# Performance work log

Measured on AMD Instinct MI355X. Metric: run time of the kernel, lower is better.

Reference implementation:

```python
import jax, jax.numpy as jnp
from jax import lax
import numpy as np

B, T, IN, H, OUT = 1024, 512, 64, 128, 2
BN_EPS = 1e-5


def _gru_layer(x, w_ih, w_hh, b_ih, b_hh):
    # x: [B, T, F]; w_ih: [3H, F]; w_hh: [3H, H]; gate order = (r, z, n) as in PyTorch
    Bb = x.shape[0]
    Hh = w_hh.shape[1]
    xg = jnp.einsum('btf,gf->btg', x, w_ih) + b_ih  # precompute input gates [B, T, 3H]

    def step(h, xg_t):
        hg = h @ w_hh.T + b_hh                       # [B, 3H]
        xr, xz, xn = jnp.split(xg_t, 3, axis=-1)
        hr, hz, hn = jnp.split(hg, 3, axis=-1)
        r = jax.nn.sigmoid(xr + hr)
        z = jax.nn.sigmoid(xz + hz)
        n = jnp.tanh(xn + r * hn)
        h_new = (1.0 - z) * n + z * h
        return h_new, h_new

    h0 = jnp.zeros((Bb, Hh), dtype=x.dtype)
    _, ys = lax.scan(step, h0, jnp.swapaxes(xg, 0, 1))  # scan over time
    return jnp.swapaxes(ys, 0, 1)                        # [B, T, H]


def setup_inputs() -> dict:
    key = jax.random.key(0)
    ks = jax.random.split(key, 16)
    s_in = 1.0 / np.sqrt(H)  # PyTorch GRU init scale
    d = {
        'x': jax.random.normal(ks[0], (B, T, IN), dtype=jnp.float32),
        'w_ih0': jax.random.uniform(ks[1], (3 * H, IN), minval=-s_in, maxval=s_in),
        'w_hh0': jax.random.uniform(ks[2], (3 * H, H), minval=-s_in, maxval=s_in),
        'b_ih0': jax.random.uniform(ks[3], (3 * H,), minval=-s_in, maxval=s_in),
        'b_hh0': jax.random.uniform(ks[4], (3 * H,), minval=-s_in, maxval=s_in),
        'w_ih1': jax.random.uniform(ks[5], (3 * H, H), minval=-s_in, maxval=s_in),
        'w_hh1': jax.random.uniform(ks[6], (3 * H, H), minval=-s_in, maxval=s_in),
        'b_ih1': jax.random.uniform(ks[7], (3 * H,), minval=-s_in, maxval=s_in),
        'b_hh1': jax.random.uniform(ks[8], (3 * H,), minval=-s_in, maxval=s_in),
        'fc1_w': jax.random.normal(ks[9], (H // 2, H)) * 0.05,
        'fc1_b': jnp.zeros((H // 2,)),
        'fc2_w': jax.random.normal(ks[10], (OUT, H // 2)) * 0.05,
        'fc2_b': jnp.zeros((OUT,)),
        'bn_gamma': jnp.ones((H // 2,)),
        'bn_beta': jnp.zeros((H // 2,)),
        'bn_mean': jnp.zeros((H // 2,)),
        'bn_var': jnp.ones((H // 2,)),
    }
    return d


def reference(x, w_ih0, w_hh0, b_ih0, b_hh0, w_ih1, w_hh1, b_ih1, b_hh1,
              fc1_w, fc1_b, fc2_w, fc2_b, bn_gamma, bn_beta, bn_mean, bn_var):
    h1 = _gru_layer(x, w_ih0, w_hh0, b_ih0, b_hh0)   # [B, T, H]
    h2 = _gru_layer(h1, w_ih1, w_hh1, b_ih1, b_hh1)  # [B, T, H]
    out = h2[:, -1, :]                                # last timestep [B, H]
    # dropout = identity (eval mode)
    out = jax.nn.relu(out @ fc1_w.T + fc1_b)          # [B, H/2]
    out = (out - bn_mean) * jax.lax.rsqrt(bn_var + BN_EPS) * bn_gamma + bn_beta
    out = out @ fc2_w.T + fc2_b                       # [B, 2]
    return out
```

## Files before the change

### kernel.cpp

```cpp
#include <hip/hip_runtime.h>
#include <hip/hip_bf16.h>

namespace {

typedef _Float16 h16;
typedef _Float16 f16x8 __attribute__((ext_vector_type(8)));
typedef _Float16 f16x4 __attribute__((ext_vector_type(4)));
typedef _Float16 f16x2 __attribute__((ext_vector_type(2)));
typedef float    f32x4 __attribute__((ext_vector_type(4)));
typedef unsigned long long u64;

constexpr int T_SEQ = 512;
constexpr int B_SZ  = 1024;
constexpr int H_DIM = 128;
constexpr int ROWS  = 16;
constexpr int NT    = 512;
constexpr int NGRP  = B_SZ / ROWS;
constexpr int CHUNK = 32;

template <int INDIM, bool PROD>
__device__ void gru_body(char* smem_raw, float* headbuf,
                         const float* __restrict__ xin,
                         const float* __restrict__ w_ih,
                         const float* __restrict__ w_hh,
                         const float* __restrict__ b_ih,
                         const float* __restrict__ b_hh,
                         u64* __restrict__ h1q,
                         int* __restrict__ flag,
                         const float* __restrict__ fc1_w,
                         const float* __restrict__ fc1_b,
                         const float* __restrict__ fc2_w,
                         const float* __restrict__ fc2_b,
                         const float* __restrict__ gamma,
                         const float* __restrict__ beta,
                         const float* __restrict__ mean,
                         const float* __restrict__ var,
                         float* __restrict__ out,
                         const int g)
{
  constexpr int KSH  = H_DIM / 32;
  constexpr int KSX  = INDIM / 32;
  constexpr int ROWP = H_DIM + INDIM + 8;

  auto hx = reinterpret_cast<h16 (*)[ROWS][ROWP]>(smem_raw);

  const int tid = threadIdx.x;
  const int wv  = tid >> 6;
  const int ln  = tid & 63;
  const int q   = ln >> 4;
  const int lr  = ln & 15;
  const int r0  = g * ROWS;
  const int j0  = wv * 16 + q * 4;

  f16x8 wA[3][KSH], wB[3][KSX];
  #pragma unroll
  for (int p = 0; p < 3; ++p) {
    const int gr = p * H_DIM + wv * 16 + lr;
    #pragma unroll
    for (int ks = 0; ks < KSH; ++ks) {
      const float* pw = w_hh + (size_t)gr * H_DIM + ks * 32 + q * 8;
      const float4 v0 = *(const float4*)(pw);
      const float4 v1 = *(const float4*)(pw + 4);
      f16x8 f;
      f[0]=(h16)v0.x; f[1]=(h16)v0.y; f[2]=(h16)v0.z; f[3]=(h16)v0.w;
      f[4]=(h16)v1.x; f[5]=(h16)v1.y; f[6]=(h16)v1.z; f[7]=(h16)v1.w;
      wA[p][ks] = f;
    }
    #pragma unroll
    for (int ks = 0; ks < KSX; ++ks) {
      const float* pw = w_ih + (size_t)gr * INDIM + ks * 32 + q * 8;
      const float4 v0 = *(const float4*)(pw);
      const float4 v1 = *(const float4*)(pw + 4);
      f16x8 f;
      f[0]=(h16)v0.x; f[1]=(h16)v0.y; f[2]=(h16)v0.z; f[3]=(h16)v0.w;
      f[4]=(h16)v1.x; f[5]=(h16)v1.y; f[6]=(h16)v1.z; f[7]=(h16)v1.w;
      wB[p][ks] = f;
    }
  }

  f32x4 bR, bZ, bNx, bNh;
  {
    const float4 ir  = *(const float4*)&b_ih[j0];
    const float4 hr  = *(const float4*)&b_hh[j0];
    const float4 iz  = *(const float4*)&b_ih[H_DIM + j0];
    const float4 hz  = *(const float4*)&b_hh[H_DIM + j0];
    const float4 in_ = *(const float4*)&b_ih[2 * H_DIM + j0];
    const float4 hn  = *(const float4*)&b_hh[2 * H_DIM + j0];
    bR[0]=ir.x+hr.x; bR[1]=ir.y+hr.y; bR[2]=ir.z+hr.z; bR[3]=ir.w+hr.w;
    bZ[0]=iz.x+hz.x; bZ[1]=iz.y+hz.y; bZ[2]=iz.z+hz.z; bZ[3]=iz.w+hz.w;
    bNx[0]=in_.x; bNx[1]=in_.y; bNx[2]=in_.z; bNx[3]=in_.w;
    bNh[0]=hn.x;  bNh[1]=hn.y;  bNh[2]=hn.z;  bNh[3]=hn.w;
  }

  const int sr = tid >> 5;
  const int si = tid & 31;

  {
    f16x4 z; z[0]=z[1]=z[2]=z[3] = (h16)0.f;
    *(f16x4*)&hx[0][sr][si * 4] = z;
  }
  f16x4 h_old; h_old[0]=h_old[1]=h_old[2]=h_old[3] = (h16)0.f;

  auto load_h1 = [&](int t, f16x4& d) {
    const u64 bits = __hip_atomic_load(&h1q[((size_t)t * NGRP + g) * 512 + tid],
                                       __ATOMIC_RELAXED, __HIP_MEMORY_SCOPE_AGENT);
    __builtin_memcpy(&d, &bits, 8);
  };

  f16x2 sA, sB;
  f16x4 cA, cB;
  if constexpr (PROD) {
    const float2 v0 = *(const float2*)(xin + ((size_t)(r0 + sr) * T_SEQ + 0) * 64 + si * 2);
    f16x2 s0; s0[0] = (h16)v0.x; s0[1] = (h16)v0.y;
    *(f16x2*)&hx[0][sr][H_DIM + si * 2] = s0;
    const float2 v1 = *(const float2*)(xin + ((size_t)(r0 + sr) * T_SEQ + 1) * 64 + si * 2);
    sA[0] = (h16)v1.x; sA[1] = (h16)v1.y;
  } else {
    while (__hip_atomic_load(flag, __ATOMIC_ACQUIRE, __HIP_MEMORY_SCOPE_AGENT) < 1)
      __builtin_amdgcn_s_sleep(2);
    f16x4 s0; load_h1(0, s0);
    *(f16x4*)&hx[0][lr][H_DIM + j0] = s0;
    load_h1(1, cA);
  }
  __syncthreads();

  auto gates = [&](const f32x4& aR, const f32x4& aZ, const f32x4& aNx2, const f32x4& aNh2,
                   f16x4& nv4, float* hnv) {
    #pragma unroll
    for (int i = 0; i < 4; ++i) {
      const float rg = __builtin_amdgcn_rcpf(1.f + __expf(-aR[i]));
      const float zg = __builtin_amdgcn_rcpf(1.f + __expf(-aZ[i]));
      const float na = aNx2[i] + rg * aNh2[i];
      const float e2 = __expf(2.f * na);
      const float ng = 1.f - 2.f * __builtin_amdgcn_rcpf(e2 + 1.f);
      const float ho = (float)h_old[i];
      const float hn = ng + zg * (ho - ng);
      hnv[i] = hn;
      nv4[i] = (h16)hn;
    }
    h_old = nv4;
  };

  auto mfma_all = [&](const f16x8* bh, const f16x8* bx,
                      f32x4& aR, f32x4& aZ, f32x4& aNh2, f32x4& aNx2) {
    aR = bR; aZ = bZ; aNh2 = bNh; aNx2 = bNx;
    #pragma unroll
    for (int ks = 0; ks < KSH; ++ks) {
      aR   = __builtin_amdgcn_mfma_f32_16x16x32_f16(wA[0][ks], bh[ks], aR, 0, 0, 0);
      aZ   = __builtin_amdgcn_mfma_f32_16x16x32_f16(wA[1][ks], bh[ks], aZ, 0, 0, 0);
      aNh2 = __builtin_amdgcn_mfma_f32_16x16x32_f16(wA[2][ks], bh[ks], aNh2, 0, 0, 0);
    }
    #pragma unroll
    for (int ks = 0; ks < KSX; ++ks) {
      aR   = __builtin_amdgcn_mfma_f32_16x16x32_f16(wB[0][ks], bx[ks], aR, 0, 0, 0);
      aZ   = __builtin_amdgcn_mfma_f32_16x16x32_f16(wB[1][ks], bx[ks], aZ, 0, 0, 0);
      aNx2 = __builtin_amdgcn_mfma_f32_16x16x32_f16(wB[2][ks], bx[ks], aNx2, 0, 0, 0);
    }
  };

  if constexpr (PROD) {
    auto pstep = [&](int t, int cur, f16x2& s_use, f16x2& s_load) {
      f16x8 bh[KSH], bx[KSX];
      #pragma unroll
      for (int ks = 0; ks < KSH; ++ks) bh[ks] = *(const f16x8*)&hx[cur][lr][ks * 32 + q * 8];
      #pragma unroll
      for (int ks = 0; ks < KSX; ++ks) bx[ks] = *(const f16x8*)&hx[cur][lr][H_DIM + ks * 32 + q * 8];

      {
        const int tt = (t + 2 < T_SEQ) ? t + 2 : T_SEQ - 1;
        const float2 v = *(const float2*)(xin + ((size_t)(r0 + sr) * T_SEQ + tt) * 64 + si * 2);
        s_load[0] = (h16)v.x; s_load[1] = (h16)v.y;
      }

      f32x4 aR, aZ, aNh2, aNx2;
      mfma_all(bh, bx, aR, aZ, aNh2, aNx2);

      f16x4 nv4; float hnv[4];
      gates(aR, aZ, aNx2, aNh2, nv4, hnv);

      u64 bits; __builtin_memcpy(&bits, &nv4, 8);
      __hip_atomic_store(&h1q[((size_t)t * NGRP + g) * 512 + tid], bits,
                         __ATOMIC_RELAXED, __HIP_MEMORY_SCOPE_AGENT);

      *(f16x4*)&hx[cur ^ 1][lr][j0] = nv4;
      *(f16x2*)&hx[cur ^ 1][sr][H_DIM + si * 2] = s_use;

      if ((t & (CHUNK - 1)) == CHUNK - 1) __threadfence();
      __syncthreads();
      if (((t & (CHUNK - 1)) == CHUNK - 1) && tid == 0)
        __hip_atomic_store(flag, (t + 1) / CHUNK, __ATOMIC_RELEASE, __HIP_MEMORY_SCOPE_AGENT);
    };

    #pragma unroll 1
    for (int t = 0; t < T_SEQ; t += 2) {
      pstep(t,     0, sA, sB);
      pstep(t + 1, 1, sB, sA);
    }
  } else {
    auto cstep = [&](int t, int cur, f16x4& s_use, f16x4& s_load) {
      f16x8 bh[KSH], bx[KSX];
      #pragma unroll
      for (int ks = 0; ks < KSH; ++ks) bh[ks] = *(const f16x8*)&hx[cur][lr][ks * 32 + q * 8];
      #pragma unroll
      for (int ks = 0; ks < KSX; ++ks) bx[ks] = *(const f16x8*)&hx[cur][lr][H_DIM + ks * 32 + q * 8];

      if (t + 2 < T_SEQ) {
        if (((t + 2) & (CHUNK - 1)) == 0) {
          const int need = (t + 2) / CHUNK + 1;
          while (__hip_atomic_load(flag, __ATOMIC_ACQUIRE, __HIP_MEMORY_SCOPE_AGENT) < need)
            __builtin_amdgcn_s_sleep(2);
        }
        load_h1(t + 2, s_load);
      }

      f32x4 aR, aZ, aNh2, aNx2;
      mfma_all(bh, bx, aR, aZ, aNh2, aNx2);

      f16x4 nv4; float hnv[4];
      gates(aR, aZ, aNx2, aNh2, nv4, hnv);

      *(f16x4*)&hx[cur ^ 1][lr][j0] = nv4;
      if (t + 1 < T_SEQ) *(f16x4*)&hx[cur ^ 1][lr][H_DIM + j0] = s_use;

      if (t == T_SEQ - 1) {
        float* h2f = headbuf;
        float* act = headbuf + 16 * 128;
        #pragma unroll
        for (int i = 0; i < 4; ++i) h2f[lr * 128 + j0 + i] = hnv[i];
        __syncthreads();
        {
          const int row = tid >> 5;
          const float* hr = &h2f[row * 128];
          #pragma unroll
          for (int half = 0; half < 2; ++half) {
            const int j = (tid & 31) + half * 32;
            float s = fc1_b[j];
            const float4* wr = (const float4*)(fc1_w + (size_t)j * H_DIM);
            #pragma unroll
            for (int k4 = 0; k4 < H_DIM / 4; ++k4) {
              const float4 w = wr[k4];
              const float4 h = ((const float4*)hr)[k4];
              s += w.x * h.x + w.y * h.y + w.z * h.z + w.w * h.w;
            }
            s = fmaxf(s, 0.f);
            s = (s - mean[j]) * rsqrtf(var[j] + 1e-5f) * gamma[j] + beta[j];
            act[row * 64 + j] = s;
          }
        }
        __syncthreads();
        if (tid < 32) {
          const int r = tid >> 1, o = tid & 1;
          float s = fc2_b[o];
          #pragma unroll
          for (int k = 0; k < 64; ++k) s += fc2_w[(size_t)o * 64 + k] * act[r * 64 + k];
          out[(size_t)(r0 + r) * 2 + o] = s;
        }
      }
      __syncthreads();
    };

    #pragma unroll 1
    for (int t = 0; t < T_SEQ; t += 2) {
      cstep(t,     0, cA, cB);
      cstep(t + 1, 1, cB, cA);
    }
  }
}

__global__ __launch_bounds__(NT, 1)
void gru_fused(const float* __restrict__ x,
               const float* __restrict__ w_ih0, const float* __restrict__ w_hh0,
               const float* __restrict__ b_ih0, const float* __restrict__ b_hh0,
               const float* __restrict__ w_ih1, const float* __restrict__ w_hh1,
               const float* __restrict__ b_ih1, const float* __restrict__ b_hh1,
               u64* __restrict__ h1q, int* __restrict__ flags,
               const float* __restrict__ fc1_w, const float* __restrict__ fc1_b,
               const float* __restrict__ fc2_w, const float* __restrict__ fc2_b,
               const float* __restrict__ gamma, const float* __restrict__ beta,
               const float* __restrict__ mean,  const float* __restrict__ var,
               float* __restrict__ out)
{
  __shared__ __align__(16) char smem[(size_t)2 * ROWS * (H_DIM + H_DIM + 8) * sizeof(h16)];
  __shared__ __align__(16) float headbuf[16 * 128 + 16 * 64];
  const int bid = blockIdx.x;
  if (bid < NGRP)
    gru_body<64, true>(smem, headbuf, x, w_ih0, w_hh0, b_ih0, b_hh0, h1q, &flags[bid],
                       nullptr, nullptr, nullptr, nullptr, nullptr, nullptr, nullptr, nullptr,
                       nullptr, bid);
  else
    gru_body<128, false>(smem, headbuf, nullptr, w_ih1, w_hh1, b_ih1, b_hh1, h1q,
                         &flags[bid - NGRP], fc1_w, fc1_b, fc2_w, fc2_b, gamma, beta,
                         mean, var, out, bid - NGRP);
}

}

extern "C" void kernel_launch(void* const* d_in, const int* in_sizes, int n_in,
                              void* d_out, int out_size, void* d_ws, size_t ws_size,
                              hipStream_t stream) {
  const float* x     = (const float*)d_in[0];
  const float* w_ih0 = (const float*)d_in[1];
  const float* w_hh0 = (const float*)d_in[2];
  const float* b_ih0 = (const float*)d_in[3];
  const float* b_hh0 = (const float*)d_in[4];
  const float* w_ih1 = (const float*)d_in[5];
  const float* w_hh1 = (const float*)d_in[6];
  const float* b_ih1 = (const float*)d_in[7];
  const float* b_hh1 = (const float*)d_in[8];
  const float* fc1_w = (const float*)d_in[9];
  const float* fc1_b = (const float*)d_in[10];
  const float* fc2_w = (const float*)d_in[11];
  const float* fc2_b = (const float*)d_in[12];
  const float* gamma = (const float*)d_in[13];
  const float* beta  = (const float*)d_in[14];
  const float* mean  = (const float*)d_in[15];
  const float* var   = (const float*)d_in[16];
  float* out = (float*)d_out;

  char* ws = (char*)d_ws;
  const size_t h1_bytes = (size_t)T_SEQ * NGRP * 512 * sizeof(u64);
  const size_t fl_bytes = (size_t)NGRP * sizeof(int);
  if (ws_size < h1_bytes + fl_bytes) return;

  u64* h1q   = (u64*)ws;
  int* flags = (int*)(ws + h1_bytes);

  hipMemsetAsync(flags, 0, fl_bytes, stream);
  gru_fused<<<dim3(2 * NGRP), dim3(NT), 0, stream>>>(
      x, w_ih0, w_hh0, b_ih0, b_hh0, w_ih1, w_hh1, b_ih1, b_hh1, h1q, flags,
      fc1_w, fc1_b, fc2_w, fc2_b, gamma, beta, mean, var, out);
}
```

Baseline: 648.2 us.

## Process two 16-row batch groups per block to interleave independent MFMA chains

```diff
diff --git a/kernel.cpp b/kernel.cpp
--- a/kernel.cpp
+++ b/kernel.cpp
@@ -16,6 +16,7 @@
 constexpr int ROWS  = 16;
 constexpr int NT    = 512;
 constexpr int NGRP  = B_SZ / ROWS;
+constexpr int NBLK  = NGRP / 2;
 constexpr int CHUNK = 32;
 
 template <int INDIM, bool PROD>
@@ -36,20 +37,22 @@
                          const float* __restrict__ mean,
                          const float* __restrict__ var,
                          float* __restrict__ out,
-                         const int g)
+                         const int gA)
 {
   constexpr int KSH  = H_DIM / 32;
   constexpr int KSX  = INDIM / 32;
   constexpr int ROWP = H_DIM + INDIM + 8;
 
-  auto hx = reinterpret_cast<h16 (*)[ROWS][ROWP]>(smem_raw);
+  auto hx = reinterpret_cast<h16 (*)[2][ROWS][ROWP]>(smem_raw);
 
   const int tid = threadIdx.x;
   const int wv  = tid >> 6;
   const int ln  = tid & 63;
   const int q   = ln >> 4;
   const int lr  = ln & 15;
-  const int r0  = g * ROWS;
+  const int gB  = gA + 1;
+  const int r0A = gA * ROWS;
+  const int r0B = gB * ROWS;
   const int j0  = wv * 16 + q * 4;
 
   f16x8 wA[3][KSH], wB[3][KSX];
@@ -97,35 +100,45 @@
 
   {
     f16x4 z; z[0]=z[1]=z[2]=z[3] = (h16)0.f;
-    *(f16x4*)&hx[0][sr][si * 4] = z;
-  }
-  f16x4 h_old; h_old[0]=h_old[1]=h_old[2]=h_old[3] = (h16)0.f;
-
-  auto load_h1 = [&](int t, f16x4& d) {
+    *(f16x4*)&hx[0][0][sr][si * 4] = z;
+    *(f16x4*)&hx[0][1][sr][si * 4] = z;
+  }
+  f16x4 h_oldA, h_oldB;
+  h_oldA[0]=h_oldA[1]=h_oldA[2]=h_oldA[3] = (h16)0.f;
+  h_oldB = h_oldA;
+
+  auto load_h1 = [&](int t, int g, f16x4& d) {
     const u64 bits = __hip_atomic_load(&h1q[((size_t)t * NGRP + g) * 512 + tid],
                                        __ATOMIC_RELAXED, __HIP_MEMORY_SCOPE_AGENT);
     __builtin_memcpy(&d, &bits, 8);
   };
-
-  f16x2 sA, sB;
-  f16x4 cA, cB;
+  auto load_x = [&](int t, int r0, f16x2& d) {
+    const int tt = (t < T_SEQ) ? t : T_SEQ - 1;
+    const float2 v = *(const float2*)(xin + ((size_t)(r0 + sr) * T_SEQ + tt) * 64 + si * 2);
+    d[0] = (h16)v.x; d[1] = (h16)v.y;
+  };
+
+  f16x2 pA_A, pA_B, pB_A, pB_B;
+  f16x4 cA_A, cA_B, cB_A, cB_B;
   if constexpr (PROD) {
-    const float2 v0 = *(const float2*)(xin + ((size_t)(r0 + sr) * T_SEQ + 0) * 64 + si * 2);
-    f16x2 s0; s0[0] = (h16)v0.x; s0[1] = (h16)v0.y;
-    *(f16x2*)&hx[0][sr][H_DIM + si * 2] = s0;
-    const float2 v1 = *(const float2*)(xin + ((size_t)(r0 + sr) * T_SEQ + 1) * 64 + si * 2);
-    sA[0] = (h16)v1.x; sA[1] = (h16)v1.y;
+    f16x2 s0;
+    load_x(0, r0A, s0); *(f16x2*)&hx[0][0][sr][H_DIM + si * 2] = s0;
+    load_x(0, r0B, s0); *(f16x2*)&hx[0][1][sr][H_DIM + si * 2] = s0;
+    load_x(1, r0A, pA_A);
+    load_x(1, r0B, pA_B);
   } else {
     while (__hip_atomic_load(flag, __ATOMIC_ACQUIRE, __HIP_MEMORY_SCOPE_AGENT) < 1)
       __builtin_amdgcn_s_sleep(2);
-    f16x4 s0; load_h1(0, s0);
-    *(f16x4*)&hx[0][lr][H_DIM + j0] = s0;
-    load_h1(1, cA);
+    f16x4 s0;
+    load_h1(0, gA, s0); *(f16x4*)&hx[0][0][lr][H_DIM + j0] = s0;
+    load_h1(0, gB, s0); *(f16x4*)&hx[0][1][lr][H_DIM + j0] = s0;
+    load_h1(1, gA, cA_A);
+    load_h1(1, gB, cA_B);
   }
   __syncthreads();
 
   auto gates = [&](const f32x4& aR, const f32x4& aZ, const f32x4& aNx2, const f32x4& aNh2,
-                   f16x4& nv4, float* hnv) {
+                   f16x4& h_old, f16x4& nv4, float* hnv) {
     #pragma unroll
     for (int i = 0; i < 4; ++i) {
       const float rg = __builtin_amdgcn_rcpf(1.f + __expf(-aR[i]));
@@ -141,49 +154,60 @@
     h_old = nv4;
   };
 
-  auto mfma_all = [&](const f16x8* bh, const f16x8* bx,
-                      f32x4& aR, f32x4& aZ, f32x4& aNh2, f32x4& aNx2) {
-    aR = bR; aZ = bZ; aNh2 = bNh; aNx2 = bNx;
-    #pragma unroll
-    for (int ks = 0; ks < KSH; ++ks) {
-      aR   = __builtin_amdgcn_mfma_f32_16x16x32_f16(wA[0][ks], bh[ks], aR, 0, 0, 0);
-      aZ   = __builtin_amdgcn_mfma_f32_16x16x32_f16(wA[1][ks], bh[ks], aZ, 0, 0, 0);
-      aNh2 = __builtin_amdgcn_mfma_f32_16x16x32_f16(wA[2][ks], bh[ks], aNh2, 0, 0, 0);
-    }
-    #pragma unroll
-    for (int ks = 0; ks < KSX; ++ks) {
-      aR   = __builtin_amdgcn_mfma_f32_16x16x32_f16(wB[0][ks], bx[ks], aR, 0, 0, 0);
-      aZ   = __builtin_amdgcn_mfma_f32_16x16x32_f16(wB[1][ks], bx[ks], aZ, 0, 0, 0);
-      aNx2 = __builtin_amdgcn_mfma_f32_16x16x32_f16(wB[2][ks], bx[ks], aNx2, 0, 0, 0);
-    }
-  };
-
   if constexpr (PROD) {
-    auto pstep = [&](int t, int cur, f16x2& s_use, f16x2& s_load) {
-      f16x8 bh[KSH], bx[KSX];
-      #pragma unroll
-      for (int ks = 0; ks < KSH; ++ks) bh[ks] = *(const f16x8*)&hx[cur][lr][ks * 32 + q * 8];
-      #pragma unroll
-      for (int ks = 0; ks < KSX; ++ks) bx[ks] = *(const f16x8*)&hx[cur][lr][H_DIM + ks * 32 + q * 8];
-
-      {
-        const int tt = (t + 2 < T_SEQ) ? t + 2 : T_SEQ - 1;
-        const float2 v = *(const float2*)(xin + ((size_t)(r0 + sr) * T_SEQ + tt) * 64 + si * 2);
-        s_load[0] = (h16)v.x; s_load[1] = (h16)v.y;
-      }
-
-      f32x4 aR, aZ, aNh2, aNx2;
-      mfma_all(bh, bx, aR, aZ, aNh2, aNx2);
-
-      f16x4 nv4; float hnv[4];
-      gates(aR, aZ, aNx2, aNh2, nv4, hnv);
-
-      u64 bits; __builtin_memcpy(&bits, &nv4, 8);
-      __hip_atomic_store(&h1q[((size_t)t * NGRP + g) * 512 + tid], bits,
+    auto pstep = [&](int t, int cur, f16x2& uA, f16x2& uB, f16x2& lA, f16x2& lB) {
+      f16x8 bhA[KSH], bxA[KSX], bhB[KSH], bxB[KSX];
+      #pragma unroll
+      for (int ks = 0; ks < KSH; ++ks) {
+        bhA[ks] = *(const f16x8*)&hx[cur][0][lr][ks * 32 + q * 8];
+        bhB[ks] = *(const f16x8*)&hx[cur][1][lr][ks * 32 + q * 8];
+      }
+      #pragma unroll
+      for (int ks = 0; ks < KSX; ++ks) {
+        bxA[ks] = *(const f16x8*)&hx[cur][0][lr][H_DIM + ks * 32 + q * 8];
+        bxB[ks] = *(const f16x8*)&hx[cur][1][lr][H_DIM + ks * 32 + q * 8];
+      }
+
+      load_x(t + 2, r0A, lA);
+      load_x(t + 2, r0B, lB);
+
+      f32x4 aRA = bR, aZA = bZ, aNhA = bNh, aNxA = bNx;
+      f32x4 aRB = bR, aZB = bZ, aNhB = bNh, aNxB = bNx;
+      #pragma unroll
+      for (int ks = 0; ks < KSH; ++ks) {
+        aRA  = __builtin_amdgcn_mfma_f32_16x16x32_f16(wA[0][ks], bhA[ks], aRA,  0, 0, 0);
+        aRB  = __builtin_amdgcn_mfma_f32_16x16x32_f16(wA[0][ks], bhB[ks], aRB,  0, 0, 0);
+        aZA  = __builtin_amdgcn_mfma_f32_16x16x32_f16(wA[1][ks], bhA[ks], aZA,  0, 0, 0);
+        aZB  = __builtin_amdgcn_mfma_f32_16x16x32_f16(wA[1][ks], bhB[ks], aZB,  0, 0, 0);
+        aNhA = __builtin_amdgcn_mfma_f32_16x16x32_f16(wA[2][ks], bhA[ks], aNhA, 0, 0, 0);
+        aNhB = __builtin_amdgcn_mfma_f32_16x16x32_f16(wA[2][ks], bhB[ks], aNhB, 0, 0, 0);
+      }
+      #pragma unroll
+      for (int ks = 0; ks < KSX; ++ks) {
+        aRA  = __builtin_amdgcn_mfma_f32_16x16x32_f16(wB[0][ks], bxA[ks], aRA,  0, 0, 0);
+        aRB  = __builtin_amdgcn_mfma_f32_16x16x32_f16(wB[0][ks], bxB[ks], aRB,  0, 0, 0);
+        aZA  = __builtin_amdgcn_mfma_f32_16x16x32_f16(wB[1][ks], bxA[ks], aZA,  0, 0, 0);
+        aZB  = __builtin_amdgcn_mfma_f32_16x16x32_f16(wB[1][ks], bxB[ks], aZB,  0, 0, 0);
+        aNxA = __builtin_amdgcn_mfma_f32_16x16x32_f16(wB[2][ks], bxA[ks], aNxA, 0, 0, 0);
+        aNxB = __builtin_amdgcn_mfma_f32_16x16x32_f16(wB[2][ks], bxB[ks], aNxB, 0, 0, 0);
+      }
+
+      f16x4 nvA, nvB; float hnA[4], hnB[4];
+      gates(aRA, aZA, aNxA, aNhA, h_oldA, nvA, hnA);
+      gates(aRB, aZB, aNxB, aNhB, h_oldB, nvB, hnB);
+
+      u64 bA, bB;
+      __builtin_memcpy(&bA, &nvA, 8);
+      __builtin_memcpy(&bB, &nvB, 8);
+      __hip_atomic_store(&h1q[((size_t)t * NGRP + gA) * 512 + tid], bA,
                          __ATOMIC_RELAXED, __HIP_MEMORY_SCOPE_AGENT);
-
-      *(f16x4*)&hx[cur ^ 1][lr][j0] = nv4;
-      *(f16x2*)&hx[cur ^ 1][sr][H_DIM + si * 2] = s_use;
+      __hip_atomic_store(&h1q[((size_t)t * NGRP + gB) * 512 + tid], bB,
+                         __ATOMIC_RELAXED, __HIP_MEMORY_SCOPE_AGENT);
+
+      *(f16x4*)&hx[cur ^ 1][0][lr][j0] = nvA;
+      *(f16x4*)&hx[cur ^ 1][1][lr][j0] = nvB;
+      *(f16x2*)&hx[cur ^ 1][0][sr][H_DIM + si * 2] = uA;
+      *(f16x2*)&hx[cur ^ 1][1][sr][H_DIM + si * 2] = uB;
 
       if ((t & (CHUNK - 1)) == CHUNK - 1) __threadfence();
       __syncthreads();
@@ -193,16 +217,22 @@
 
     #pragma unroll 1
     for (int t = 0; t < T_SEQ; t += 2) {
-      pstep(t,     0, sA, sB);
-      pstep(t + 1, 1, sB, sA);
+      pstep(t,     0, pA_A, pA_B, pB_A, pB_B);
+      pstep(t + 1, 1, pB_A, pB_B, pA_A, pA_B);
     }
   } else {
-    auto cstep = [&](int t, int cur, f16x4& s_use, f16x4& s_load) {
-      f16x8 bh[KSH], bx[KSX];
-      #pragma unroll
-      for (int ks = 0; ks < KSH; ++ks) bh[ks] = *(const f16x8*)&hx[cur][lr][ks * 32 + q * 8];
-      #pragma unroll
-      for (int ks = 0; ks < KSX; ++ks) bx[ks] = *(const f16x8*)&hx[cur][lr][H_DIM + ks * 32 + q * 8];
+    auto cstep = [&](int t, int cur, f16x4& uA, f16x4& uB, f16x4& lA, f16x4& lB) {
+      f16x8 bhA[KSH], bxA[KSX], bhB[KSH], bxB[KSX];
+      #pragma unroll
+      for (int ks = 0; ks < KSH; ++ks) {
+        bhA[ks] = *(const f16x8*)&hx[cur][0][lr][ks * 32 + q * 8];
+        bhB[ks] = *(const f16x8*)&hx[cur][1][lr][ks * 32 + q * 8];
+      }
+      #pragma unroll
+      for (int ks = 0; ks < KSX; ++ks) {
+        bxA[ks] = *(const f16x8*)&hx[cur][0][lr][H_DIM + ks * 32 + q * 8];
+        bxB[ks] = *(const f16x8*)&hx[cur][1][lr][H_DIM + ks * 32 + q * 8];
+      }
 
       if (t + 2 < T_SEQ) {
         if (((t + 2) & (CHUNK - 1)) == 0) {
@@ -210,50 +240,76 @@
           while (__hip_atomic_load(flag, __ATOMIC_ACQUIRE, __HIP_MEMORY_SCOPE_AGENT) < need)
             __builtin_amdgcn_s_sleep(2);
         }
-        load_h1(t + 2, s_load);
-      }
-
-      f32x4 aR, aZ, aNh2, aNx2;
-      mfma_all(bh, bx, aR, aZ, aNh2, aNx2);
-
-      f16x4 nv4; float hnv[4];
-      gates(aR, aZ, aNx2, aNh2, nv4, hnv);
-
-      *(f16x4*)&hx[cur ^ 1][lr][j0] = nv4;
-      if (t + 1 < T_SEQ) *(f16x4*)&hx[cur ^ 1][lr][H_DIM + j0] = s_use;
+        load_h1(t + 2, gA, lA);
+        load_h1(t + 2, gB, lB);
+      }
+
+      f32x4 aRA = bR, aZA = bZ, aNhA = bNh, aNxA = bNx;
+      f32x4 aRB = bR, aZB = bZ, aNhB = bNh, aNxB = bNx;
+      #pragma unroll
+      for (int ks = 0; ks < KSH; ++ks) {
+        aRA  = __builtin_amdgcn_mfma_f32_16x16x32_f16(wA[0][ks], bhA[ks], aRA,  0, 0, 0);
+        aRB  = __builtin_amdgcn_mfma_f32_16x16x32_f16(wA[0][ks], bhB[ks], aRB,  0, 0, 0);
+        aZA  = __builtin_amdgcn_mfma_f32_16x16x32_f16(wA[1][ks], bhA[ks], aZA,  0, 0, 0);
+        aZB  = __builtin_amdgcn_mfma_f32_16x16x32_f16(wA[1][ks], bhB[ks], aZB,  0, 0, 0);
+        aNhA = __builtin_amdgcn_mfma_f32_16x16x32_f16(wA[2][ks], bhA[ks], aNhA, 0, 0, 0);
+        aNhB = __builtin_amdgcn_mfma_f32_16x16x32_f16(wA[2][ks], bhB[ks], aNhB, 0, 0, 0);
+      }
+      #pragma unroll
+      for (int ks = 0; ks < KSX; ++ks) {
+        aRA  = __builtin_amdgcn_mfma_f32_16x16x32_f16(wB[0][ks], bxA[ks], aRA,  0, 0, 0);
+        aRB  = __builtin_amdgcn_mfma_f32_16x16x32_f16(wB[0][ks], bxB[ks], aRB,  0, 0, 0);
+        aZA  = __builtin_amdgcn_mfma_f32_16x16x32_f16(wB[1][ks], bxA[ks], aZA,  0, 0, 0);
+        aZB  = __builtin_amdgcn_mfma_f32_16x16x32_f16(wB[1][ks], bxB[ks], aZB,  0, 0, 0);
+        aNxA = __builtin_amdgcn_mfma_f32_16x16x32_f16(wB[2][ks], bxA[ks], aNxA, 0, 0, 0);
+        aNxB = __builtin_amdgcn_mfma_f32_16x16x32_f16(wB[2][ks], bxB[ks], aNxB, 0, 0, 0);
+      }
+
+      f16x4 nvA, nvB; float hnA[4], hnB[4];
+      gates(aRA, aZA, aNxA, aNhA, h_oldA, nvA, hnA);
+      gates(aRB, aZB, aNxB, aNhB, h_oldB, nvB, hnB);
+
+      *(f16x4*)&hx[cur ^ 1][0][lr][j0] = nvA;
+      *(f16x4*)&hx[cur ^ 1][1][lr][j0] = nvB;
+      if (t + 1 < T_SEQ) {
+        *(f16x4*)&hx[cur ^ 1][0][lr][H_DIM + j0] = uA;
+        *(f16x4*)&hx[cur ^ 1][1][lr][H_DIM + j0] = uB;
+      }
 
       if (t == T_SEQ - 1) {
         float* h2f = headbuf;
-        float* act = headbuf + 16 * 128;
+        float* act = headbuf + 32 * 128;
         #pragma unroll
-        for (int i = 0; i < 4; ++i) h2f[lr * 128 + j0 + i] = hnv[i];
-        __syncthreads();
-        {
-          const int row = tid >> 5;
-          const float* hr = &h2f[row * 128];
-          #pragma unroll
-          for (int half = 0; half < 2; ++half) {
-            const int j = (tid & 31) + half * 32;
-            float s = fc1_b[j];
-            const float4* wr = (const float4*)(fc1_w + (size_t)j * H_DIM);
-            #pragma unroll
-            for (int k4 = 0; k4 < H_DIM / 4; ++k4) {
-              const float4 w = wr[k4];
-              const float4 h = ((const float4*)hr)[k4];
-              s += w.x * h.x + w.y * h.y + w.z * h.z + w.w * h.w;
-            }
-            s = fmaxf(s, 0.f);
-            s = (s - mean[j]) * rsqrtf(var[j] + 1e-5f) * gamma[j] + beta[j];
-            act[row * 64 + j] = s;
-          }
+        for (int i = 0; i < 4; ++i) {
+          h2f[lr * 128 + j0 + i]        = hnA[i];
+          h2f[(16 + lr) * 128 + j0 + i] = hnB[i];
         }
         __syncthreads();
-        if (tid < 32) {
+        #pragma unroll
+        for (int rep = 0; rep < 4; ++rep) {
+          const int task = rep * NT + tid;
+          const int row  = task >> 6;
+          const int j    = task & 63;
+          float s = fc1_b[j];
+          const float4* wr = (const float4*)(fc1_w + (size_t)j * H_DIM);
+          const float*  hr = &h2f[row * 128];
+          #pragma unroll
+          for (int k4 = 0; k4 < H_DIM / 4; ++k4) {
+            const float4 w = wr[k4];
+            const float4 h = ((const float4*)hr)[k4];
+            s += w.x * h.x + w.y * h.y + w.z * h.z + w.w * h.w;
+          }
+          s = fmaxf(s, 0.f);
+          s = (s - mean[j]) * rsqrtf(var[j] + 1e-5f) * gamma[j] + beta[j];
+          act[row * 64 + j] = s;
+        }
+        __syncthreads();
+        if (tid < 64) {
           const int r = tid >> 1, o = tid & 1;
           float s = fc2_b[o];
           #pragma unroll
           for (int k = 0; k < 64; ++k) s += fc2_w[(size_t)o * 64 + k] * act[r * 64 + k];
-          out[(size_t)(r0 + r) * 2 + o] = s;
+          out[(size_t)(r0A + r) * 2 + o] = s;
         }
       }
       __syncthreads();
@@ -261,8 +317,8 @@
 
     #pragma unroll 1
     for (int t = 0; t < T_SEQ; t += 2) {
-      cstep(t,     0, cA, cB);
-      cstep(t + 1, 1, cB, cA);
+      cstep(t,     0, cA_A, cA_B, cB_A, cB_B);
+      cstep(t + 1, 1, cB_A, cB_B, cA_A, cA_B);
     }
   }
 }
@@ -280,17 +336,17 @@
                const float* __restrict__ mean,  const float* __restrict__ var,
                float* __restrict__ out)
 {
-  __shared__ __align__(16) char smem[(size_t)2 * ROWS * (H_DIM + H_DIM + 8) * sizeof(h16)];
-  __shared__ __align__(16) float headbuf[16 * 128 + 16 * 64];
+  __shared__ __align__(16) char smem[(size_t)2 * 2 * ROWS * (H_DIM + H_DIM + 8) * sizeof(h16)];
+  __shared__ __align__(16) float headbuf[32 * 128 + 32 * 64];
   const int bid = blockIdx.x;
-  if (bid < NGRP)
+  if (bid < NBLK)
     gru_body<64, true>(smem, headbuf, x, w_ih0, w_hh0, b_ih0, b_hh0, h1q, &flags[bid],
                        nullptr, nullptr, nullptr, nullptr, nullptr, nullptr, nullptr, nullptr,
-                       nullptr, bid);
+                       nullptr, 2 * bid);
   else
     gru_body<128, false>(smem, headbuf, nullptr, w_ih1, w_hh1, b_ih1, b_hh1, h1q,
-                         &flags[bid - NGRP], fc1_w, fc1_b, fc2_w, fc2_b, gamma, beta,
-                         mean, var, out, bid - NGRP);
+                         &flags[bid - NBLK], fc1_w, fc1_b, fc2_w, fc2_b, gamma, beta,
+                         mean, var, out, 2 * (bid - NBLK));
 }
 
 }
@@ -319,14 +375,14 @@
 
   char* ws = (char*)d_ws;
   const size_t h1_bytes = (size_t)T_SEQ * NGRP * 512 * sizeof(u64);
-  const size_t fl_bytes = (size_t)NGRP * sizeof(int);
+  const size_t fl_bytes = (size_t)NBLK * sizeof(int);
   if (ws_size < h1_bytes + fl_bytes) return;
 
   u64* h1q   = (u64*)ws;
   int* flags = (int*)(ws + h1_bytes);
 
   hipMemsetAsync(flags, 0, fl_bytes, stream);
-  gru_fused<<<dim3(2 * NGRP), dim3(NT), 0, stream>>>(
+  gru_fused<<<dim3(2 * NBLK), dim3(NT), 0, stream>>>(
       x, w_ih0, w_hh0, b_ih0, b_hh0, w_ih1, w_hh1, b_ih1, b_hh1, h1q, flags,
       fc1_w, fc1_b, fc2_w, fc2_b, gamma, beta, mean, var, out);
 }
```

Result: slower. 1.051 ms (+62.1%).
